# Kernel optimization log

Hardware: AMD Instinct MI355X
Metric: run time of the kernel (lower is better)

## Reference

```python
import jax, jax.numpy as jnp
import numpy as np

N_NODES, N_EDGES = 50000, 800000
IN_CH, HID, HEADS, OUT_CH = 128, 64, 4, 2
NEG_SLOPE = 0.2
EPS = 1e-16


def setup_inputs() -> dict:
    key = jax.random.key(0)
    ks = jax.random.split(key, 16)
    def rn(k, shape, scale=0.1):
        return jax.random.normal(k, shape, dtype=jnp.float32) * scale
    inp = {
        "x": jax.random.normal(ks[0], (N_NODES, IN_CH), dtype=jnp.float32),
        "edge_index": jax.random.randint(ks[1], (2, N_EDGES), 0, N_NODES, dtype=jnp.int64),
        "stats": jax.random.normal(ks[2], (N_EDGES, 3), dtype=jnp.float32),
        # conv1: GATConv(IN_CH -> HID, heads=HEADS, concat=True)
        "W1": rn(ks[3], (IN_CH, HEADS * HID)),
        "att_src1": rn(ks[4], (HEADS, HID)),
        "att_dst1": rn(ks[5], (HEADS, HID)),
        "b1": rn(ks[6], (HEADS * HID,)),
        # conv2: GATConv(HEADS*HID -> HID, heads=1, concat=False)
        "W2": rn(ks[7], (HEADS * HID, HID)),
        "att_src2": rn(ks[8], (1, HID)),
        "att_dst2": rn(ks[9], (1, HID)),
        "b2": rn(ks[10], (HID,)),
        # edge MLP: Linear(2*HID+3 -> HID) -> ReLU -> Linear(HID -> OUT_CH)
        "mW1": rn(ks[11], (2 * HID + 3, HID)),
        "mb1": rn(ks[12], (HID,)),
        "mW2": rn(ks[13], (HID, OUT_CH)),
        "mb2": rn(ks[14], (OUT_CH,)),
    }
    return inp


def gat_layer(x, src, dst, W, att_s, att_d, n_nodes):
    """PyG GATConv core: per-edge attention, softmax over destination, scatter-add."""
    H, C = att_s.shape
    h = (x @ W).reshape(n_nodes, H, C)                      # [N,H,C]
    a_s = jnp.sum(h * att_s, axis=-1)                        # [N,H]
    a_d = jnp.sum(h * att_d, axis=-1)                        # [N,H]
    e = a_s[src] + a_d[dst]                                  # [E,H]
    e = jnp.where(e > 0, e, NEG_SLOPE * e)                   # leaky_relu
    m = jax.ops.segment_max(e, dst, num_segments=n_nodes)    # [N,H]
    m = jnp.where(jnp.isfinite(m), m, 0.0)
    e = jnp.exp(e - m[dst])
    s = jax.ops.segment_sum(e, dst, num_segments=n_nodes)    # [N,H]
    alpha = e / (s[dst] + EPS)                               # [E,H]
    out = jax.ops.segment_sum(alpha[:, :, None] * h[src], dst, num_segments=n_nodes)
    return out                                               # [N,H,C]


def reference(x, edge_index, stats, W1, att_src1, att_dst1, b1,
              W2, att_src2, att_dst2, b2, mW1, mb1, mW2, mb2):
    n = x.shape[0]
    row, col = edge_index[0], edge_index[1]
    # add self loops (PyG GATConv default)
    loop = jnp.arange(n, dtype=edge_index.dtype)
    src = jnp.concatenate([row, loop])
    dst = jnp.concatenate([col, loop])

    # conv1: heads concatenated, then ELU (dropout disabled at inference)
    h1 = gat_layer(x, src, dst, W1, att_src1, att_dst1, n)
    h1 = h1.reshape(n, HEADS * HID) + b1
    h1 = jax.nn.elu(h1)

    # conv2: single head, concat=False (mean over 1 head == squeeze)
    h2 = gat_layer(h1, src, dst, W2, att_src2, att_dst2, n)
    node_emb = h2[:, 0, :] + b2                              # [N,HID]

    # edge MLP over gathered endpoint embeddings + per-edge stats
    feat = jnp.concatenate([node_emb[row], node_emb[col], stats], axis=1)  # [E,2*HID+3]
    hidden = jax.nn.relu(feat @ mW1 + mb1)
    return hidden @ mW2 + mb2                                # [E,OUT_CH]
```

## Files before the change

kernel.cpp:

```cpp
#include <hip/hip_runtime.h>
#include <math.h>

#define NN 50000
#define NE 800000
#define EP (NE + NN)
#define INC 128
#define HID 64
#define HEADS 4
#define C1 (HEADS * HID)
#define NEG 0.2f
#define EPSS 1e-16f

#define SCHUNK 512
#define NSB ((NN + SCHUNK - 1) / SCHUNK)

#define KP1 136
#define KP2 264
typedef __attribute__((ext_vector_type(8))) short bf16x8;
typedef __attribute__((ext_vector_type(4))) float f32x4;

__device__ __forceinline__ unsigned short f2bf(float f) {
    unsigned u = __float_as_uint(f);
    unsigned r = (u + 0x7FFFu + ((u >> 16) & 1u)) >> 16;
    return (unsigned short)r;
}
__device__ __forceinline__ float bf2f(unsigned short b) {
    return __uint_as_float(((unsigned)b) << 16);
}

__global__ __launch_bounds__(SCHUNK) void scan_partial(const int* __restrict__ counts,
                                                       int* __restrict__ bsum) {
    __shared__ int lds[SCHUNK];
    int i = blockIdx.x * SCHUNK + threadIdx.x;
    lds[threadIdx.x] = (i < NN) ? counts[i] : 0;
    __syncthreads();
    for (int off = SCHUNK / 2; off > 0; off >>= 1) {
        if (threadIdx.x < off) lds[threadIdx.x] += lds[threadIdx.x + off];
        __syncthreads();
    }
    if (threadIdx.x == 0) bsum[blockIdx.x] = lds[0];
}

__global__ void scan_top(int* __restrict__ bsum, int* __restrict__ rowptr) {
    __shared__ int lds[NSB];
    int t = threadIdx.x;
    if (t < NSB) lds[t] = bsum[t];
    __syncthreads();
    if (t == 0) {
        int acc = 0;
        for (int i = 0; i < NSB; ++i) { int v = lds[i]; lds[i] = acc; acc += v; }
        rowptr[NN] = acc;
    }
    __syncthreads();
    if (t < NSB) bsum[t] = lds[t];
}

__global__ __launch_bounds__(SCHUNK) void scan_final(const int* __restrict__ counts,
                                                     const int* __restrict__ bsum,
                                                     int* __restrict__ rowptr,
                                                     int* __restrict__ cursor) {
    __shared__ int lds[SCHUNK];
    int i = blockIdx.x * SCHUNK + threadIdx.x;
    int v = (i < NN) ? counts[i] : 0;
    lds[threadIdx.x] = v;
    __syncthreads();
    for (int off = 1; off < SCHUNK; off <<= 1) {
        int t = (threadIdx.x >= off) ? lds[threadIdx.x - off] : 0;
        __syncthreads();
        lds[threadIdx.x] += t;
        __syncthreads();
    }
    if (i < NN) {
        int excl = lds[threadIdx.x] - v + bsum[blockIdx.x];
        rowptr[i] = excl;
        cursor[i] = excl;
    }
}

__global__ void csr_fill(const int* __restrict__ ei, int* __restrict__ cursor,
                         int* __restrict__ csr_src, int* __restrict__ csr_dst) {
    int e = blockIdx.x * 256 + threadIdx.x;
    if (e >= EP) return;
    int s, d;
    if (e < NE) { s = ei[e]; d = ei[NE + e]; } else { s = d = e - NE; }
    int pos = atomicAdd(&cursor[d], 1);
    csr_src[pos] = s;
    csr_dst[pos] = d;
}

#define PREP_N0 (C1 * INC)
#define PREP_N1 (HID * C1)
#define PREP_N2 (5 * 4 * 64 * 8)
#define PREP_N3 1024
#define PREP_N4 (NN * INC)
#define PREP_TOT (PREP_N0 + PREP_N1 + PREP_N2 + PREP_N3 + PREP_N4)
__global__ void prep_all(const float* __restrict__ mW1, const float* __restrict__ W1,
                         const float* __restrict__ W2, const int* __restrict__ ei,
                         const float* __restrict__ x,
                         const float* __restrict__ att_s1, const float* __restrict__ att_d1,
                         unsigned short* __restrict__ w1h, unsigned short* __restrict__ w1l,
                         unsigned short* __restrict__ w2h, unsigned short* __restrict__ w2l,
                         unsigned short* __restrict__ wFh, unsigned short* __restrict__ wFl,
                         float* __restrict__ vsd, unsigned short* __restrict__ xb,
                         int* __restrict__ counts) {
    int i = blockIdx.x * 256 + threadIdx.x;
    if (i < PREP_N0) {
        int c = i >> 7, k = i & 127;
        float f = W1[k * C1 + c];
        unsigned short h = f2bf(f);
        w1h[i] = h; w1l[i] = f2bf(f - bf2f(h));
        return;
    }
    i -= PREP_N0;
    if (i < PREP_N1) {
        int c = i >> 8, k = i & 255;
        float f = W2[k * HID + c];
        unsigned short h = f2bf(f);
        w2h[i] = h; w2l[i] = f2bf(f - bf2f(h));
        return;
    }
    i -= PREP_N1;
    if (i < PREP_N2) {
        int kk = i >> 11;
        int ct = (i >> 9) & 3;
        int l  = (i >> 3) & 63;
        int j  = i & 7;
        int cl = l & 15, g = l >> 4;
        int k   = kk * 32 + g * 8 + j;
        int col = ct * 16 + cl;
        unsigned short h = 0, lo = 0;
        if (k < 131) {
            float f = mW1[k * 64 + col];
            h  = f2bf(f);
            lo = f2bf(f - bf2f(h));
        }
        wFh[i] = h;
        wFl[i] = lo;
        return;
    }
    i -= PREP_N2;
    if (i < PREP_N3) {
        int type = i >> 9;
        int rem  = i & 511;
        int h = rem >> 7, k = rem & 127;
        const float* att = type ? att_d1 : att_s1;
        float acc = 0.f;
        for (int c = 0; c < 64; ++c)
            acc += W1[k * C1 + h * 64 + c] * att[h * 64 + c];
        vsd[i] = acc;
        return;
    }
    i -= PREP_N3;
    if (i < PREP_N4) {
        xb[i] = f2bf(x[i]);
        return;
    }
    i -= PREP_N4;
    if (i < EP) {
        int d = (i < NE) ? ei[NE + i] : (i - NE);
        atomicAdd(&counts[d], 1);
    }
}

__global__ __launch_bounds__(256) void att1_kernel(const float* __restrict__ x,
                                                   const float* __restrict__ vsd,
                                                   float* __restrict__ as1,
                                                   float* __restrict__ ad1) {
    __shared__ float vsS[1024];
    const int tid = threadIdx.x;
    for (int idx = tid; idx < 1024; idx += 256) vsS[idx] = vsd[idx];
    __syncthreads();

    const int n = blockIdx.x * 16 + (tid >> 4);
    const int l16 = tid & 15;
    const float* xp = x + (size_t)n * INC + l16 * 8;
    float4 xa = *(const float4*)xp;
    float4 xc = *(const float4*)(xp + 4);

    float o[8];
#pragma unroll
    for (int h = 0; h < 4; ++h) {
        const float* vp = vsS + h * 128 + l16 * 8;
        const float* dp = vsS + 512 + h * 128 + l16 * 8;
        o[h]     = xa.x * vp[0] + xa.y * vp[1] + xa.z * vp[2] + xa.w * vp[3]
                 + xc.x * vp[4] + xc.y * vp[5] + xc.z * vp[6] + xc.w * vp[7];
        o[4 + h] = xa.x * dp[0] + xa.y * dp[1] + xa.z * dp[2] + xa.w * dp[3]
                 + xc.x * dp[4] + xc.y * dp[5] + xc.z * dp[6] + xc.w * dp[7];
    }
#pragma unroll
    for (int off = 1; off < 16; off <<= 1)
#pragma unroll
        for (int v = 0; v < 8; ++v) o[v] += __shfl_xor(o[v], off);
    if (l16 == 0) {
        *(float4*)(as1 + n * 4) = make_float4(o[0], o[1], o[2], o[3]);
        *(float4*)(ad1 + n * 4) = make_float4(o[4], o[5], o[6], o[7]);
    }
}

__global__ void edge_w1k(const int* __restrict__ csr_src, const int* __restrict__ csr_dst,
                         const float* __restrict__ as1, const float* __restrict__ ad1,
                         float* __restrict__ w1e) {
    int i = blockIdx.x * 256 + threadIdx.x;
    if (i >= EP) return;
    int s = csr_src[i], d = csr_dst[i];
    float4 a = *(const float4*)(as1 + s * 4);
    float4 b = *(const float4*)(ad1 + d * 4);
    float4 o;
    float t;
    t = a.x + b.x; t = t > 0.f ? t : NEG * t; o.x = __expf(t);
    t = a.y + b.y; t = t > 0.f ? t : NEG * t; o.y = __expf(t);
    t = a.z + b.z; t = t > 0.f ? t : NEG * t; o.z = __expf(t);
    t = a.w + b.w; t = t > 0.f ? t : NEG * t; o.w = __expf(t);
    *(float4*)(w1e + (size_t)i * 4) = o;
}

__global__ void edge_w2k(const int* __restrict__ csr_src, const int* __restrict__ csr_dst,
                         const float* __restrict__ as2, const float* __restrict__ ad2,
                         float* __restrict__ w2e) {
    int i = blockIdx.x * 256 + threadIdx.x;
    if (i >= EP) return;
    float t = as2[csr_src[i]] + ad2[csr_dst[i]];
    t = t > 0.f ? t : NEG * t;
    w2e[i] = __expf(t);
}

__global__ __launch_bounds__(256) void conv1_agg(const int* __restrict__ rowptr,
                                                 const int* __restrict__ csr_src,
                                                 const float* __restrict__ w1e,
                                                 const unsigned short* __restrict__ xb,
                                                 unsigned short* __restrict__ xaggb) {
    const int tid = threadIdx.x;
    const int node = blockIdx.x * 16 + (tid >> 4);
    const int l16 = tid & 15;
    const int beg = rowptr[node], end = rowptr[node + 1];

    float acc[4][8];
#pragma unroll
    for (int h = 0; h < 4; ++h)
#pragma unroll
        for (int j = 0; j < 8; ++j) acc[h][j] = 0.f;
    float sm[4] = {0.f, 0.f, 0.f, 0.f};

#pragma unroll 2
    for (int i = beg; i < end; ++i) {
        int s = csr_src[i];
        float4 w = *(const float4*)(w1e + (size_t)i * 4);
        bf16x8 xv = *(const bf16x8*)(xb + (size_t)s * INC + l16 * 8);
        float xf[8];
#pragma unroll
        for (int j = 0; j < 8; ++j) xf[j] = bf2f((unsigned short)xv[j]);
#pragma unroll
        for (int j = 0; j < 8; ++j) {
            acc[0][j] += w.x * xf[j];
            acc[1][j] += w.y * xf[j];
            acc[2][j] += w.z * xf[j];
            acc[3][j] += w.w * xf[j];
        }
        sm[0] += w.x; sm[1] += w.y; sm[2] += w.z; sm[3] += w.w;
    }

#pragma unroll
    for (int h = 0; h < 4; ++h) {
        const float rden = 1.f / (sm[h] + EPSS);
        bf16x8 ob;
#pragma unroll
        for (int j = 0; j < 8; ++j) ob[j] = (short)f2bf(acc[h][j] * rden);
        *(bf16x8*)(xaggb + ((size_t)node * 4 + h) * INC + l16 * 8) = ob;
    }
}

__global__ __launch_bounds__(256) void gemm1b(const unsigned short* __restrict__ xaggb,
                                              const unsigned short* __restrict__ w1h,
                                              const unsigned short* __restrict__ w1l,
                                              const float* __restrict__ b1,
                                              unsigned short* __restrict__ h1c) {
    __shared__ unsigned short wH[64 * KP1];
    __shared__ unsigned short wL[64 * KP1];
    const int tid = threadIdx.x;
    const int n0 = blockIdx.x * 64;
    const int q  = blockIdx.y;

    for (int idx = tid; idx < 64 * 16; idx += 256) {
        int col = idx >> 4, ch = idx & 15;
        *(bf16x8*)(wH + col * KP1 + ch * 8) =
            *(const bf16x8*)(w1h + ((q * 64 + col) << 7) + ch * 8);
        *(bf16x8*)(wL + col * KP1 + ch * 8) =
            *(const bf16x8*)(w1l + ((q * 64 + col) << 7) + ch * 8);
    }

    const int w = tid >> 6, l = tid & 63;
    const int cl = l & 15, g = l >> 4, g8 = g * 8;
    const int na = min(n0 + w * 16 + cl, NN - 1);

    bf16x8 aH[4];
#pragma unroll
    for (int kk = 0; kk < 4; ++kk)
        aH[kk] = *(const bf16x8*)(xaggb + ((size_t)na * 4 + q) * INC + kk * 32 + g8);

    f32x4 acc[4];
#pragma unroll
    for (int ct = 0; ct < 4; ++ct) acc[ct] = (f32x4){0.f, 0.f, 0.f, 0.f};

    __syncthreads();

#pragma unroll
    for (int kk = 0; kk < 4; ++kk) {
        const int ko = kk * 32 + g8;
#pragma unroll
        for (int ct = 0; ct < 4; ++ct) {
            const bf16x8 bH = *(const bf16x8*)(wH + (ct * 16 + cl) * KP1 + ko);
            const bf16x8 bL = *(const bf16x8*)(wL + (ct * 16 + cl) * KP1 + ko);
            acc[ct] = __builtin_amdgcn_mfma_f32_16x16x32_bf16(aH[kk], bH, acc[ct], 0, 0, 0);
            acc[ct] = __builtin_amdgcn_mfma_f32_16x16x32_bf16(aH[kk], bL, acc[ct], 0, 0, 0);
        }
    }

#pragma unroll
    for (int reg = 0; reg < 4; ++reg) {
        const int nd = n0 + w * 16 + g * 4 + reg;
        if (nd < NN) {
#pragma unroll
            for (int ct = 0; ct < 4; ++ct) {
                const int col = q * 64 + ct * 16 + cl;
                float o = acc[ct][reg] + b1[col];
                o = o > 0.f ? o : (__expf(o) - 1.f);
                h1c[(size_t)nd * C1 + col] = f2bf(o);
            }
        }
    }
}

__global__ __launch_bounds__(256) void gemm2_mfma(const unsigned short* __restrict__ h1c,
                                                  const unsigned short* __restrict__ w2h,
                                                  const unsigned short* __restrict__ w2l,
                                                  const float* __restrict__ att_s,
                                                  const float* __restrict__ att_d,
                                                  unsigned short* __restrict__ h2b,
                                                  float* __restrict__ as2,
                                                  float* __restrict__ ad2) {
    __shared__ unsigned short wH[64 * KP2];
    __shared__ unsigned short wL[64 * KP2];
    const int tid = threadIdx.x;
    const int n0 = blockIdx.x * 64;

    for (int idx = tid; idx < 64 * 32; idx += 256) {
        int col = idx >> 5, ch = idx & 31;
        *(bf16x8*)(wH + col * KP2 + ch * 8) =
            *(const bf16x8*)(w2h + ((col) << 8) + ch * 8);
        *(bf16x8*)(wL + col * KP2 + ch * 8) =
            *(const bf16x8*)(w2l + ((col) << 8) + ch * 8);
    }

    const int w = tid >> 6, l = tid & 63;
    const int cl = l & 15, g = l >> 4, g8 = g * 8;
    const int na = min(n0 + w * 16 + cl, NN - 1);

    f32x4 acc[4];
#pragma unroll
    for (int ct = 0; ct < 4; ++ct) acc[ct] = (f32x4){0.f, 0.f, 0.f, 0.f};

    __syncthreads();

#pragma unroll
    for (int kk = 0; kk < 8; ++kk) {
        const bf16x8 aH = *(const bf16x8*)(h1c + (size_t)na * C1 + kk * 32 + g8);
        const int ko = kk * 32 + g8;
#pragma unroll
        for (int ct = 0; ct < 4; ++ct) {
            const bf16x8 bH = *(const bf16x8*)(wH + (ct * 16 + cl) * KP2 + ko);
            const bf16x8 bL = *(const bf16x8*)(wL + (ct * 16 + cl) * KP2 + ko);
            acc[ct] = __builtin_amdgcn_mfma_f32_16x16x32_bf16(aH, bH, acc[ct], 0, 0, 0);
            acc[ct] = __builtin_amdgcn_mfma_f32_16x16x32_bf16(aH, bL, acc[ct], 0, 0, 0);
        }
    }

    float asc[4], adc[4];
#pragma unroll
    for (int ct = 0; ct < 4; ++ct) {
        asc[ct] = att_s[ct * 16 + cl];
        adc[ct] = att_d[ct * 16 + cl];
    }

#pragma unroll
    for (int reg = 0; reg < 4; ++reg) {
        const int nd = n0 + w * 16 + g * 4 + reg;
        float sa = 0.f, sd = 0.f;
#pragma unroll
        for (int ct = 0; ct < 4; ++ct) {
            sa += acc[ct][reg] * asc[ct];
            sd += acc[ct][reg] * adc[ct];
        }
#pragma unroll
        for (int off = 8; off > 0; off >>= 1) {
            sa += __shfl_xor(sa, off);
            sd += __shfl_xor(sd, off);
        }
        if (nd < NN) {
#pragma unroll
            for (int ct = 0; ct < 4; ++ct)
                h2b[(size_t)nd * HID + ct * 16 + cl] = f2bf(acc[ct][reg]);
            if (cl == 0) { as2[nd] = sa; ad2[nd] = sd; }
        }
    }
}

__global__ __launch_bounds__(256) void conv2_agg(const int* __restrict__ rowptr,
                                                 const int* __restrict__ csr_src,
                                                 const float* __restrict__ w2e,
                                                 const unsigned short* __restrict__ h2b,
                                                 const float* __restrict__ b2,
                                                 unsigned short* __restrict__ embb) {
    const int tid  = threadIdx.x;
    const int wid  = tid >> 6;
    const int l    = tid & 63;
    const int half = l >> 5;
    const int l32  = l & 31;
    const int node = blockIdx.x * 8 + wid * 2 + half;
    const int beg = rowptr[node], end = rowptr[node + 1];

    float a0 = 0.f, a1 = 0.f, sm = 0.f;
#pragma unroll 2
    for (int i = beg; i < end; ++i) {
        int s = csr_src[i];
        float w = w2e[i];
        unsigned hv = *(const unsigned*)(h2b + (size_t)s * HID + l32 * 2);
        a0 += w * bf2f((unsigned short)(hv & 0xFFFF));
        a1 += w * bf2f((unsigned short)(hv >> 16));
        sm += w;
    }
    const float rden = 1.f / (sm + EPSS);
    float o0 = a0 * rden + b2[l32 * 2];
    float o1 = a1 * rden + b2[l32 * 2 + 1];
    unsigned outw = (unsigned)f2bf(o0) | ((unsigned)f2bf(o1) << 16);
    *(unsigned*)(embb + (size_t)node * HID + l32 * 2) = outw;
}

__global__ __launch_bounds__(512) void edge_mlp_mfma(const int* __restrict__ ei,
                                                     const unsigned short* __restrict__ embb,
                                                     const float* __restrict__ stats,
                                                     const unsigned short* __restrict__ wFh,
                                                     const unsigned short* __restrict__ wFl,
                                                     const float* __restrict__ mb1,
                                                     const float* __restrict__ mW2,
                                                     const float* __restrict__ mb2,
                                                     float* __restrict__ out) {
    __shared__ unsigned short sH[PREP_N2];
    __shared__ unsigned short sL[PREP_N2];
    __shared__ float biaS[64], w2aS[64], w2bS[64];
    const int tid = threadIdx.x;
    for (int idx = tid; idx < PREP_N2 / 8; idx += 512) {
        ((float4*)sH)[idx] = ((const float4*)wFh)[idx];
        ((float4*)sL)[idx] = ((const float4*)wFl)[idx];
    }
    if (tid < 64) {
        biaS[tid] = mb1[tid];
        w2aS[tid] = mW2[tid * 2];
        w2bS[tid] = mW2[tid * 2 + 1];
    }

    const int l  = tid & 63;
    const int cl = l & 15;
    const int g  = l >> 4;
    const int g8 = g * 8;
    const float ob0 = mb2[0], ob1 = mb2[1];

    const int t = blockIdx.x * 8 + (tid >> 6);

    bf16x8 a[2][5];
#pragma unroll
    for (int s = 0; s < 2; ++s) {
        const int ge_a = t * 32 + s * 16 + cl;
        const int rn = ei[ge_a];
        const int cn = ei[NE + ge_a];
        const unsigned short* rp = embb + (size_t)rn * HID;
        const unsigned short* cp = embb + (size_t)cn * HID;
        a[s][0] = *(const bf16x8*)(rp + g8);
        a[s][1] = *(const bf16x8*)(rp + 32 + g8);
        a[s][2] = *(const bf16x8*)(cp + g8);
        a[s][3] = *(const bf16x8*)(cp + 32 + g8);
        bf16x8 z = {0, 0, 0, 0, 0, 0, 0, 0};
        if (g == 0) {
            const float* sp = stats + (size_t)ge_a * 3;
            z[0] = (short)f2bf(sp[0]);
            z[1] = (short)f2bf(sp[1]);
            z[2] = (short)f2bf(sp[2]);
        }
        a[s][4] = z;
    }

    f32x4 acc[2][4];
#pragma unroll
    for (int s = 0; s < 2; ++s)
#pragma unroll
        for (int ct = 0; ct < 4; ++ct)
            acc[s][ct] = (f32x4){0.f, 0.f, 0.f, 0.f};

    __syncthreads();

#pragma unroll
    for (int kk = 0; kk < 5; ++kk) {
#pragma unroll
        for (int ct = 0; ct < 4; ++ct) {
            const int fo = ((kk * 4 + ct) * 64 + l) * 8;
            const bf16x8 wHf = *(const bf16x8*)(sH + fo);
            const bf16x8 wLf = *(const bf16x8*)(sL + fo);
#pragma unroll
            for (int s = 0; s < 2; ++s) {
                acc[s][ct] = __builtin_amdgcn_mfma_f32_16x16x32_bf16(wHf, a[s][kk], acc[s][ct], 0, 0, 0);
                acc[s][ct] = __builtin_amdgcn_mfma_f32_16x16x32_bf16(wLf, a[s][kk], acc[s][ct], 0, 0, 0);
            }
        }
    }

#pragma unroll
    for (int s = 0; s < 2; ++s) {
        float p0 = 0.f, p1 = 0.f;
#pragma unroll
        for (int ct = 0; ct < 4; ++ct) {
            const int hb = ct * 16 + g * 4;
            float4 bi = *(const float4*)(biaS + hb);
            float4 wa = *(const float4*)(w2aS + hb);
            float4 wb = *(const float4*)(w2bS + hb);
#pragma unroll
            for (int reg = 0; reg < 4; ++reg) {
                float bv = (reg == 0) ? bi.x : (reg == 1) ? bi.y : (reg == 2) ? bi.z : bi.w;
                float av = (reg == 0) ? wa.x : (reg == 1) ? wa.y : (reg == 2) ? wa.z : wa.w;
                float wv = (reg == 0) ? wb.x : (reg == 1) ? wb.y : (reg == 2) ? wb.z : wb.w;
                float h = fmaxf(acc[s][ct][reg] + bv, 0.f);
                p0 += h * av;
                p1 += h * wv;
            }
        }
        p0 += __shfl_xor(p0, 16); p0 += __shfl_xor(p0, 32);
        p1 += __shfl_xor(p1, 16); p1 += __shfl_xor(p1, 32);
        if (g == 0) {
            const int ge = t * 32 + s * 16 + cl;
            *(float2*)(out + (size_t)ge * 2) = make_float2(p0 + ob0, p1 + ob1);
        }
    }
}

extern "C" void kernel_launch(void* const* d_in, const int* in_sizes, int n_in,
                              void* d_out, int out_size, void* d_ws, size_t ws_size,
                              hipStream_t stream) {
    const float* x      = (const float*)d_in[0];
    const int*   ei     = (const int*)d_in[1];
    const float* stats  = (const float*)d_in[2];
    const float* W1     = (const float*)d_in[3];
    const float* att_s1 = (const float*)d_in[4];
    const float* att_d1 = (const float*)d_in[5];
    const float* b1     = (const float*)d_in[6];
    const float* W2     = (const float*)d_in[7];
    const float* att_s2 = (const float*)d_in[8];
    const float* att_d2 = (const float*)d_in[9];
    const float* b2     = (const float*)d_in[10];
    const float* mW1    = (const float*)d_in[11];
    const float* mb1    = (const float*)d_in[12];
    const float* mW2    = (const float*)d_in[13];
    const float* mb2    = (const float*)d_in[14];
    float* out = (float*)d_out;
    float* ws  = (float*)d_ws;

    int*   rowptr  = (int*)ws;
    int*   csr_src = rowptr + NN + 16;
    int*   csr_dst = csr_src + EP;
    float* as1     = (float*)(csr_dst + EP);
    float* ad1     = as1 + (size_t)4 * NN;
    unsigned short* xb    = (unsigned short*)(ad1 + (size_t)4 * NN);
    unsigned short* xaggb = xb + (size_t)128 * NN;
    unsigned short* h1c   = xaggb + (size_t)512 * NN;
    unsigned short* h2b   = h1c + (size_t)256 * NN;
    unsigned short* embb  = h2b + (size_t)64 * NN;
    float* as2     = (float*)(embb + (size_t)64 * NN);
    float* ad2     = as2 + NN;
    unsigned short* w1h = (unsigned short*)(ad2 + NN);
    unsigned short* w1l = w1h + C1 * INC;
    unsigned short* w2h = w1l + C1 * INC;
    unsigned short* w2l = w2h + HID * C1;
    unsigned short* wFh = w2l + HID * C1;
    unsigned short* wFl = wFh + PREP_N2;
    float* vsd     = (float*)(wFl + PREP_N2);
    float* w1e     = vsd + 1024;
    float* w2e     = w1e + (size_t)4 * EP;
    int*   counts  = (int*)(w2e + EP + 64);
    int*   bsum    = counts + NN + 64;
    int*   cursor  = bsum + NSB + 64;

    hipMemsetAsync(counts, 0, NN * sizeof(int), stream);
    prep_all<<<(PREP_TOT + EP + 255) / 256, 256, 0, stream>>>(
        mW1, W1, W2, ei, x, att_s1, att_d1,
        w1h, w1l, w2h, w2l, wFh, wFl, vsd, xb, counts);
    scan_partial<<<NSB, SCHUNK, 0, stream>>>(counts, bsum);
    scan_top<<<1, 128, 0, stream>>>(bsum, rowptr);
    scan_final<<<NSB, SCHUNK, 0, stream>>>(counts, bsum, rowptr, cursor);
    csr_fill<<<(EP + 255) / 256, 256, 0, stream>>>(ei, cursor, csr_src, csr_dst);

    att1_kernel<<<NN / 16, 256, 0, stream>>>(x, vsd, as1, ad1);
    edge_w1k<<<(EP + 255) / 256, 256, 0, stream>>>(csr_src, csr_dst, as1, ad1, w1e);
    conv1_agg<<<NN / 16, 256, 0, stream>>>(rowptr, csr_src, w1e, xb, xaggb);
    gemm1b<<<dim3((NN + 63) / 64, 4), 256, 0, stream>>>(xaggb, w1h, w1l, b1, h1c);

    gemm2_mfma<<<(NN + 63) / 64, 256, 0, stream>>>(h1c, w2h, w2l, att_s2, att_d2,
                                                   h2b, as2, ad2);
    edge_w2k<<<(EP + 255) / 256, 256, 0, stream>>>(csr_src, csr_dst, as2, ad2, w2e);
    conv2_agg<<<NN / 8, 256, 0, stream>>>(rowptr, csr_src, w2e, h2b, b2, embb);

    edge_mlp_mfma<<<(NE / 32) / 8, 512, 0, stream>>>(ei, embb, stats, wFh, wFl,
                                                     mb1, mW2, mb2, out);
}
```

Before: 308.7 us.

## Interleave CSR src/dst into int2 and amortize edge MLP weight staging over tiles

CSR source and destination arrays are merged into a single int2 array, so csr_fill does one 8-byte store and edge_w1k/edge_w2k do one 8-byte load per edge. The aggregation kernels now read only .x from that interleaved array, which doubles the bytes they stream for source indices. The edge MLP kernel now has each wave process four 32-edge tiles in a loop, and launches a quarter as many blocks. The aim is to spread the LDS weight staging and block setup over more work, at the cost of fewer blocks in flight.

```diff
diff --git a/kernel.cpp b/kernel.cpp
--- a/kernel.cpp
+++ b/kernel.cpp
@@ -78,14 +78,13 @@
 }
 
 __global__ void csr_fill(const int* __restrict__ ei, int* __restrict__ cursor,
-                         int* __restrict__ csr_src, int* __restrict__ csr_dst) {
+                         int2* __restrict__ csr2) {
     int e = blockIdx.x * 256 + threadIdx.x;
     if (e >= EP) return;
     int s, d;
     if (e < NE) { s = ei[e]; d = ei[NE + e]; } else { s = d = e - NE; }
     int pos = atomicAdd(&cursor[d], 1);
-    csr_src[pos] = s;
-    csr_dst[pos] = d;
+    csr2[pos] = make_int2(s, d);
 }
 
 #define PREP_N0 (C1 * INC)
@@ -197,14 +196,14 @@
     }
 }
 
-__global__ void edge_w1k(const int* __restrict__ csr_src, const int* __restrict__ csr_dst,
+__global__ void edge_w1k(const int2* __restrict__ csr2,
                          const float* __restrict__ as1, const float* __restrict__ ad1,
                          float* __restrict__ w1e) {
     int i = blockIdx.x * 256 + threadIdx.x;
     if (i >= EP) return;
-    int s = csr_src[i], d = csr_dst[i];
-    float4 a = *(const float4*)(as1 + s * 4);
-    float4 b = *(const float4*)(ad1 + d * 4);
+    int2 sd = csr2[i];
+    float4 a = *(const float4*)(as1 + sd.x * 4);
+    float4 b = *(const float4*)(ad1 + sd.y * 4);
     float4 o;
     float t;
     t = a.x + b.x; t = t > 0.f ? t : NEG * t; o.x = __expf(t);
@@ -214,18 +213,19 @@
     *(float4*)(w1e + (size_t)i * 4) = o;
 }
 
-__global__ void edge_w2k(const int* __restrict__ csr_src, const int* __restrict__ csr_dst,
+__global__ void edge_w2k(const int2* __restrict__ csr2,
                          const float* __restrict__ as2, const float* __restrict__ ad2,
                          float* __restrict__ w2e) {
     int i = blockIdx.x * 256 + threadIdx.x;
     if (i >= EP) return;
-    float t = as2[csr_src[i]] + ad2[csr_dst[i]];
+    int2 sd = csr2[i];
+    float t = as2[sd.x] + ad2[sd.y];
     t = t > 0.f ? t : NEG * t;
     w2e[i] = __expf(t);
 }
 
 __global__ __launch_bounds__(256) void conv1_agg(const int* __restrict__ rowptr,
-                                                 const int* __restrict__ csr_src,
+                                                 const int2* __restrict__ csr2,
                                                  const float* __restrict__ w1e,
                                                  const unsigned short* __restrict__ xb,
                                                  unsigned short* __restrict__ xaggb) {
@@ -243,7 +243,7 @@
 
 #pragma unroll 2
     for (int i = beg; i < end; ++i) {
-        int s = csr_src[i];
+        int s = csr2[i].x;
         float4 w = *(const float4*)(w1e + (size_t)i * 4);
         bf16x8 xv = *(const bf16x8*)(xb + (size_t)s * INC + l16 * 8);
         float xf[8];
@@ -405,7 +405,7 @@
 }
 
 __global__ __launch_bounds__(256) void conv2_agg(const int* __restrict__ rowptr,
-                                                 const int* __restrict__ csr_src,
+                                                 const int2* __restrict__ csr2,
                                                  const float* __restrict__ w2e,
                                                  const unsigned short* __restrict__ h2b,
                                                  const float* __restrict__ b2,
@@ -421,7 +421,7 @@
     float a0 = 0.f, a1 = 0.f, sm = 0.f;
 #pragma unroll 2
     for (int i = beg; i < end; ++i) {
-        int s = csr_src[i];
+        int s = csr2[i].x;
         float w = w2e[i];
         unsigned hv = *(const unsigned*)(h2b + (size_t)s * HID + l32 * 2);
         a0 += w * bf2f((unsigned short)(hv & 0xFFFF));
@@ -435,6 +435,7 @@
     *(unsigned*)(embb + (size_t)node * HID + l32 * 2) = outw;
 }
 
+#define NT_MLP (NE / 32)
 __global__ __launch_bounds__(512) void edge_mlp_mfma(const int* __restrict__ ei,
                                                      const unsigned short* __restrict__ embb,
                                                      const float* __restrict__ stats,
@@ -457,85 +458,88 @@
         w2aS[tid] = mW2[tid * 2];
         w2bS[tid] = mW2[tid * 2 + 1];
     }
+    __syncthreads();
 
     const int l  = tid & 63;
     const int cl = l & 15;
     const int g  = l >> 4;
     const int g8 = g * 8;
     const float ob0 = mb2[0], ob1 = mb2[1];
-
-    const int t = blockIdx.x * 8 + (tid >> 6);
-
-    bf16x8 a[2][5];
-#pragma unroll
-    for (int s = 0; s < 2; ++s) {
-        const int ge_a = t * 32 + s * 16 + cl;
-        const int rn = ei[ge_a];
-        const int cn = ei[NE + ge_a];
-        const unsigned short* rp = embb + (size_t)rn * HID;
-        const unsigned short* cp = embb + (size_t)cn * HID;
-        a[s][0] = *(const bf16x8*)(rp + g8);
-        a[s][1] = *(const bf16x8*)(rp + 32 + g8);
-        a[s][2] = *(const bf16x8*)(cp + g8);
-        a[s][3] = *(const bf16x8*)(cp + 32 + g8);
-        bf16x8 z = {0, 0, 0, 0, 0, 0, 0, 0};
-        if (g == 0) {
-            const float* sp = stats + (size_t)ge_a * 3;
-            z[0] = (short)f2bf(sp[0]);
-            z[1] = (short)f2bf(sp[1]);
-            z[2] = (short)f2bf(sp[2]);
-        }
-        a[s][4] = z;
-    }
-
-    f32x4 acc[2][4];
-#pragma unroll
-    for (int s = 0; s < 2; ++s)
-#pragma unroll
-        for (int ct = 0; ct < 4; ++ct)
-            acc[s][ct] = (f32x4){0.f, 0.f, 0.f, 0.f};
-
-    __syncthreads();
-
-#pragma unroll
-    for (int kk = 0; kk < 5; ++kk) {
-#pragma unroll
-        for (int ct = 0; ct < 4; ++ct) {
-            const int fo = ((kk * 4 + ct) * 64 + l) * 8;
-            const bf16x8 wHf = *(const bf16x8*)(sH + fo);
-            const bf16x8 wLf = *(const bf16x8*)(sL + fo);
-#pragma unroll
-            for (int s = 0; s < 2; ++s) {
-                acc[s][ct] = __builtin_amdgcn_mfma_f32_16x16x32_bf16(wHf, a[s][kk], acc[s][ct], 0, 0, 0);
-                acc[s][ct] = __builtin_amdgcn_mfma_f32_16x16x32_bf16(wLf, a[s][kk], acc[s][ct], 0, 0, 0);
+    const int tbase = (blockIdx.x * 8 + (tid >> 6)) * 4;
+
+    for (int tt = 0; tt < 4; ++tt) {
+        const int t = tbase + tt;
+        if (t >= NT_MLP) break;
+
+        bf16x8 a[2][5];
+#pragma unroll
+        for (int s = 0; s < 2; ++s) {
+            const int ge_a = t * 32 + s * 16 + cl;
+            const int rn = ei[ge_a];
+            const int cn = ei[NE + ge_a];
+            const unsigned short* rp = embb + (size_t)rn * HID;
+            const unsigned short* cp = embb + (size_t)cn * HID;
+            a[s][0] = *(const bf16x8*)(rp + g8);
+            a[s][1] = *(const bf16x8*)(rp + 32 + g8);
+            a[s][2] = *(const bf16x8*)(cp + g8);
+            a[s][3] = *(const bf16x8*)(cp + 32 + g8);
+            bf16x8 z = {0, 0, 0, 0, 0, 0, 0, 0};
+            if (g == 0) {
+                const float* sp = stats + (size_t)ge_a * 3;
+                z[0] = (short)f2bf(sp[0]);
+                z[1] = (short)f2bf(sp[1]);
+                z[2] = (short)f2bf(sp[2]);
             }
-        }
-    }
-
-#pragma unroll
-    for (int s = 0; s < 2; ++s) {
-        float p0 = 0.f, p1 = 0.f;
-#pragma unroll
-        for (int ct = 0; ct < 4; ++ct) {
-            const int hb = ct * 16 + g * 4;
-            float4 bi = *(const float4*)(biaS + hb);
-            float4 wa = *(const float4*)(w2aS + hb);
-            float4 wb = *(const float4*)(w2bS + hb);
-#pragma unroll
-            for (int reg = 0; reg < 4; ++reg) {
-                float bv = (reg == 0) ? bi.x : (reg == 1) ? bi.y : (reg == 2) ? bi.z : bi.w;
-                float av = (reg == 0) ? wa.x : (reg == 1) ? wa.y : (reg == 2) ? wa.z : wa.w;
-                float wv = (reg == 0) ? wb.x : (reg == 1) ? wb.y : (reg == 2) ? wb.z : wb.w;
-                float h = fmaxf(acc[s][ct][reg] + bv, 0.f);
-                p0 += h * av;
-                p1 += h * wv;
+            a[s][4] = z;
+        }
+
+        f32x4 acc[2][4];
+#pragma unroll
+        for (int s = 0; s < 2; ++s)
+#pragma unroll
+            for (int ct = 0; ct < 4; ++ct)
+                acc[s][ct] = (f32x4){0.f, 0.f, 0.f, 0.f};
+
+#pragma unroll
+        for (int kk = 0; kk < 5; ++kk) {
+#pragma unroll
+            for (int ct = 0; ct < 4; ++ct) {
+                const int fo = ((kk * 4 + ct) * 64 + l) * 8;
+                const bf16x8 wHf = *(const bf16x8*)(sH + fo);
+                const bf16x8 wLf = *(const bf16x8*)(sL + fo);
+#pragma unroll
+                for (int s = 0; s < 2; ++s) {
+                    acc[s][ct] = __builtin_amdgcn_mfma_f32_16x16x32_bf16(wHf, a[s][kk], acc[s][ct], 0, 0, 0);
+                    acc[s][ct] = __builtin_amdgcn_mfma_f32_16x16x32_bf16(wLf, a[s][kk], acc[s][ct], 0, 0, 0);
+                }
             }
         }
-        p0 += __shfl_xor(p0, 16); p0 += __shfl_xor(p0, 32);
-        p1 += __shfl_xor(p1, 16); p1 += __shfl_xor(p1, 32);
-        if (g == 0) {
-            const int ge = t * 32 + s * 16 + cl;
-            *(float2*)(out + (size_t)ge * 2) = make_float2(p0 + ob0, p1 + ob1);
+
+#pragma unroll
+        for (int s = 0; s < 2; ++s) {
+            float p0 = 0.f, p1 = 0.f;
+#pragma unroll
+            for (int ct = 0; ct < 4; ++ct) {
+                const int hb = ct * 16 + g * 4;
+                float4 bi = *(const float4*)(biaS + hb);
+                float4 wa = *(const float4*)(w2aS + hb);
+                float4 wb = *(const float4*)(w2bS + hb);
+#pragma unroll
+                for (int reg = 0; reg < 4; ++reg) {
+                    float bv = (reg == 0) ? bi.x : (reg == 1) ? bi.y : (reg == 2) ? bi.z : bi.w;
+                    float av = (reg == 0) ? wa.x : (reg == 1) ? wa.y : (reg == 2) ? wa.z : wa.w;
+                    float wv = (reg == 0) ? wb.x : (reg == 1) ? wb.y : (reg == 2) ? wb.z : wb.w;
+                    float h = fmaxf(acc[s][ct][reg] + bv, 0.f);
+                    p0 += h * av;
+                    p1 += h * wv;
+                }
+            }
+            p0 += __shfl_xor(p0, 16); p0 += __shfl_xor(p0, 32);
+            p1 += __shfl_xor(p1, 16); p1 += __shfl_xor(p1, 32);
+            if (g == 0) {
+                const int ge = t * 32 + s * 16 + cl;
+                *(float2*)(out + (size_t)ge * 2) = make_float2(p0 + ob0, p1 + ob1);
+            }
         }
     }
 }
@@ -562,9 +566,8 @@
     float* ws  = (float*)d_ws;
 
     int*   rowptr  = (int*)ws;
-    int*   csr_src = rowptr + NN + 16;
-    int*   csr_dst = csr_src + EP;
-    float* as1     = (float*)(csr_dst + EP);
+    int2*  csr2    = (int2*)(rowptr + NN + 16);
+    float* as1     = (float*)(csr2 + EP);
     float* ad1     = as1 + (size_t)4 * NN;
     unsigned short* xb    = (unsigned short*)(ad1 + (size_t)4 * NN);
     unsigned short* xaggb = xb + (size_t)128 * NN;
@@ -593,18 +596,18 @@
     scan_partial<<<NSB, SCHUNK, 0, stream>>>(counts, bsum);
     scan_top<<<1, 128, 0, stream>>>(bsum, rowptr);
     scan_final<<<NSB, SCHUNK, 0, stream>>>(counts, bsum, rowptr, cursor);
-    csr_fill<<<(EP + 255) / 256, 256, 0, stream>>>(ei, cursor, csr_src, csr_dst);
+    csr_fill<<<(EP + 255) / 256, 256, 0, stream>>>(ei, cursor, csr2);
 
     att1_kernel<<<NN / 16, 256, 0, stream>>>(x, vsd, as1, ad1);
-    edge_w1k<<<(EP + 255) / 256, 256, 0, stream>>>(csr_src, csr_dst, as1, ad1, w1e);
-    conv1_agg<<<NN / 16, 256, 0, stream>>>(rowptr, csr_src, w1e, xb, xaggb);
+    edge_w1k<<<(EP + 255) / 256, 256, 0, stream>>>(csr2, as1, ad1, w1e);
+    conv1_agg<<<NN / 16, 256, 0, stream>>>(rowptr, csr2, w1e, xb, xaggb);
     gemm1b<<<dim3((NN + 63) / 64, 4), 256, 0, stream>>>(xaggb, w1h, w1l, b1, h1c);
 
     gemm2_mfma<<<(NN + 63) / 64, 256, 0, stream>>>(h1c, w2h, w2l, att_s2, att_d2,
                                                    h2b, as2, ad2);
-    edge_w2k<<<(EP + 255) / 256, 256, 0, stream>>>(csr_src, csr_dst, as2, ad2, w2e);
-    conv2_agg<<<NN / 8, 256, 0, stream>>>(rowptr, csr_src, w2e, h2b, b2, embb);
-
-    edge_mlp_mfma<<<(NE / 32) / 8, 512, 0, stream>>>(ei, embb, stats, wFh, wFl,
-                                                     mb1, mW2, mb2, out);
-}
+    edge_w2k<<<(EP + 255) / 256, 256, 0, stream>>>(csr2, as2, ad2, w2e);
+    conv2_agg<<<NN / 8, 256, 0, stream>>>(rowptr, csr2, w2e, h2b, b2, embb);
+
+    edge_mlp_mfma<<<(NT_MLP + 31) / 32, 512, 0, stream>>>(ei, embb, stats, wFh, wFl,
+                                                          mb1, mW2, mb2, out);
+}
```

Measured after the change: 316.3 us. 2.5% more time.
